# Performance work log

Measured on AMD Instinct MI355X. Metric: run time of the kernel, lower is better.

The kernel has to match this reference:

```python
import jax, jax.numpy as jnp
import numpy as np

N_NODES = 80000
N_EDGES = 1280000
N_GRAPHS = 256
NEG_SLOPE = 0.2


def _edge_softmax(alpha, dst, n):
    # PyG softmax over incoming edges per target node, with 1e-16 eps
    m = jax.ops.segment_max(alpha, dst, num_segments=n)          # [N,H]
    e = jnp.exp(alpha - m[dst])
    s = jax.ops.segment_sum(e, dst, num_segments=n)              # [N,H]
    return e / (s[dst] + 1e-16)


def _gat_layer(x, src, dst, W, a_src, a_dst, b, heads, out_ch):
    n = x.shape[0]
    h = (x @ W).reshape(n, heads, out_ch)                        # [N,H,C]
    al_src = (h * a_src).sum(-1)                                 # [N,H]
    al_dst = (h * a_dst).sum(-1)                                 # [N,H]
    alpha = jax.nn.leaky_relu(al_src[src] + al_dst[dst], NEG_SLOPE)  # [E,H]
    alpha = _edge_softmax(alpha, dst, n)
    out = jax.ops.segment_sum(h[src] * alpha[:, :, None], dst, num_segments=n)
    return out.reshape(n, heads * out_ch) + b


def setup_inputs() -> dict:
    key = jax.random.key(0)
    ks = jax.random.split(key, 16)
    x = jax.random.normal(ks[0], (N_NODES, 9), dtype=jnp.float32)
    edge_index = jax.random.randint(ks[1], (2, N_EDGES), 0, N_NODES, dtype=jnp.int64)
    batch = jnp.sort(jax.random.randint(ks[2], (N_NODES,), 0, N_GRAPHS, dtype=jnp.int64))
    s = 0.1
    p = {}
    p['W1'] = jax.random.normal(ks[3], (9, 3 * 45), dtype=jnp.float32) * s
    p['a_src1'] = jax.random.normal(ks[4], (3, 45), dtype=jnp.float32) * s
    p['a_dst1'] = jax.random.normal(ks[5], (3, 45), dtype=jnp.float32) * s
    p['b1'] = jnp.zeros((3 * 45,), dtype=jnp.float32)
    p['W2'] = jax.random.normal(ks[6], (135, 3 * 18), dtype=jnp.float32) * s
    p['a_src2'] = jax.random.normal(ks[7], (3, 18), dtype=jnp.float32) * s
    p['a_dst2'] = jax.random.normal(ks[8], (3, 18), dtype=jnp.float32) * s
    p['b2'] = jnp.zeros((3 * 18,), dtype=jnp.float32)
    p['W3'] = jax.random.normal(ks[9], (54, 4), dtype=jnp.float32) * s
    p['a_src3'] = jax.random.normal(ks[10], (1, 4), dtype=jnp.float32) * s
    p['a_dst3'] = jax.random.normal(ks[11], (1, 4), dtype=jnp.float32) * s
    p['b3'] = jnp.zeros((4,), dtype=jnp.float32)
    return dict(x=x, edge_index=edge_index, batch=batch, **p)


def reference(x, edge_index, batch,
              W1, a_src1, a_dst1, b1,
              W2, a_src2, a_dst2, b2,
              W3, a_src3, a_dst3, b3):
    n = x.shape[0]
    # GATConv default: add self-loops once (same structure every layer)
    loop = jnp.arange(n, dtype=edge_index.dtype)
    src = jnp.concatenate([edge_index[0], loop])
    dst = jnp.concatenate([edge_index[1], loop])

    h = _gat_layer(x, src, dst, W1, a_src1, a_dst1, b1, 3, 45)
    h = jax.nn.relu(h)  # dropout is identity in eval mode
    h = _gat_layer(h, src, dst, W2, a_src2, a_dst2, b2, 3, 18)
    h = jax.nn.relu(h)
    h = _gat_layer(h, src, dst, W3, a_src3, a_dst3, b3, 1, 4)

    g = jax.ops.segment_max(h, batch, num_segments=N_GRAPHS)  # global_max_pool
    g = jnp.where(jnp.isneginf(g), jnp.float32(-1e9), g)      # guard empty graphs
    return jax.nn.log_softmax(g, axis=1)
```

## Files before the change

### kernel.cpp

```cpp
#include <hip/hip_runtime.h>
#include <hip/hip_bf16.h>

#define N_NODES 80000
#define N_EDGES 1280000
#define E_TOT   (N_EDGES + N_NODES)
#define N_GRAPHS 256
#define NEG_SLOPE 0.2f

__device__ __forceinline__ float leaky(float a) { return fmaxf(a, NEG_SLOPE * a); }

template <int H>
__device__ __forceinline__ float pick(const float (&arr)[H], int h) {
    float r = arr[0];
    #pragma unroll
    for (int j = 1; j < H; ++j) r = (h == j) ? arr[j] : r;
    return r;
}

__device__ __forceinline__ unsigned f2mono(float f) {
    unsigned u = __float_as_uint(f);
    return u ^ ((u >> 31) ? 0xFFFFFFFFu : 0x80000000u);
}
__device__ __forceinline__ float mono2f(unsigned u) {
    u = (u & 0x80000000u) ? (u ^ 0x80000000u) : ~u;
    return __uint_as_float(u);
}

__global__ void k_init(int* __restrict__ counts, int* __restrict__ fill,
                       unsigned* __restrict__ genc) {
    int i = blockIdx.x * blockDim.x + threadIdx.x;
    if (i < N_NODES) { counts[i] = 0; fill[i] = 0; }
    if (i < N_GRAPHS * 4) genc[i] = f2mono(-1e9f);
}

__global__ void k_hist(const int* __restrict__ dst, int* __restrict__ counts) {
    int i = blockIdx.x * blockDim.x + threadIdx.x;
    if (i >= E_TOT) return;
    int d = (i < N_EDGES) ? dst[i] : (i - N_EDGES);
    atomicAdd(&counts[d], 1);
}

#define SCAN_B 256
__global__ void k_scan_block(const int* __restrict__ counts, int* __restrict__ rp,
                             int* __restrict__ bsum, int n) {
    __shared__ int sa[SCAN_B], sb[SCAN_B];
    int tid = threadIdx.x;
    int gi = blockIdx.x * SCAN_B + tid;
    int v = (gi < n) ? counts[gi] : 0;
    sa[tid] = v;
    __syncthreads();
    int* cur = sa; int* nxt = sb;
    #pragma unroll
    for (int d = 1; d < SCAN_B; d <<= 1) {
        int t = cur[tid];
        if (tid >= d) t += cur[tid - d];
        nxt[tid] = t;
        __syncthreads();
        int* tmp = cur; cur = nxt; nxt = tmp;
    }
    if (gi < n) rp[gi] = cur[tid] - v;
    if (tid == SCAN_B - 1) bsum[blockIdx.x] = cur[tid];
}

__global__ void k_scan_tops(const int* __restrict__ bsum, int* __restrict__ boff, int nb) {
    __shared__ int sa[512], sb[512];
    int tid = threadIdx.x;
    int v = (tid < nb) ? bsum[tid] : 0;
    sa[tid] = v;
    __syncthreads();
    int* cur = sa; int* nxt = sb;
    #pragma unroll
    for (int d = 1; d < 512; d <<= 1) {
        int t = cur[tid];
        if (tid >= d) t += cur[tid - d];
        nxt[tid] = t;
        __syncthreads();
        int* tmp = cur; cur = nxt; nxt = tmp;
    }
    if (tid < nb) boff[tid] = cur[tid] - v;
}

__global__ void k_scan_add_pre1(int* __restrict__ rp, const int* __restrict__ boff,
                                const float* __restrict__ x, const float* __restrict__ W1,
                                const float* __restrict__ as1, const float* __restrict__ ad1,
                                float* __restrict__ als, float* __restrict__ ald, int n) {
    __shared__ float ps[27], pd[27];
    int t = threadIdx.x;
    int gi = blockIdx.x * blockDim.x + t;
    if (gi < n) rp[gi] += boff[blockIdx.x];
    if (gi == 0) rp[n] = E_TOT;
    if (t < 27) {
        int h = t / 9, k = t % 9;
        float s = 0.f, d = 0.f;
        for (int c = 0; c < 45; ++c) {
            float w = W1[k * 135 + h * 45 + c];
            s += w * as1[h * 45 + c];
            d += w * ad1[h * 45 + c];
        }
        ps[t] = s; pd[t] = d;
    }
    __syncthreads();
    if (gi >= n) return;
    float xr[9];
    #pragma unroll
    for (int k = 0; k < 9; ++k) xr[k] = x[gi * 9 + k];
    #pragma unroll
    for (int h = 0; h < 3; ++h) {
        float s = 0.f, d = 0.f;
        #pragma unroll
        for (int k = 0; k < 9; ++k) { s += xr[k] * ps[h * 9 + k]; d += xr[k] * pd[h * 9 + k]; }
        als[gi * 3 + h] = s;
        ald[gi * 3 + h] = d;
    }
}

__global__ void k_scatter(const int* __restrict__ src, const int* __restrict__ dst,
                          const int* __restrict__ rp, int* __restrict__ fill,
                          int* __restrict__ srcs) {
    int i = blockIdx.x * blockDim.x + threadIdx.x;
    if (i >= E_TOT) return;
    int s, d;
    if (i < N_EDGES) { s = src[i]; d = dst[i]; }
    else             { s = i - N_EDGES; d = s; }
    int pos = rp[d] + atomicAdd(&fill[d], 1);
    srcs[pos] = s;
}

__global__ void k_agg1x(const int* __restrict__ rp, const int* __restrict__ srcs,
                        const float* __restrict__ x, const float* __restrict__ als,
                        const float* __restrict__ ald, float* __restrict__ wv,
                        float* __restrict__ aggx, int n) {
    int wid = threadIdx.x >> 6, lane = threadIdx.x & 63;
    int node = blockIdx.x * (blockDim.x >> 6) + wid;
    if (node >= n) return;
    int beg = rp[node], end = rp[node + 1];

    float aldv[3];
    #pragma unroll
    for (int h = 0; h < 3; ++h) aldv[h] = ald[node * 3 + h];

    float ss[3] = {0.f, 0.f, 0.f};
    for (int i = beg + lane; i < end; i += 64) {
        int s = srcs[i];
        #pragma unroll
        for (int h = 0; h < 3; ++h) {
            float e = __expf(leaky(als[s * 3 + h] + aldv[h]));
            wv[i * 3 + h] = e;
            ss[h] += e;
        }
    }
    #pragma unroll
    for (int h = 0; h < 3; ++h) {
        #pragma unroll
        for (int off = 32; off; off >>= 1) ss[h] += __shfl_xor(ss[h], off, 64);
    }
    float inv[3];
    #pragma unroll
    for (int h = 0; h < 3; ++h) inv[h] = 1.f / (ss[h] + 1e-16f);

    int es = lane >> 5, li = lane & 31;
    int lic = li < 27 ? li : 26;
    int hh = lic / 9;
    int kk = lic % 9;
    float invh = pick(inv, hh);

    float acc = 0.f;
    int i = beg + es;
    for (; i + 14 < end; i += 16) {
        int s0 = srcs[i],      s1 = srcs[i + 2],  s2 = srcs[i + 4],  s3 = srcs[i + 6];
        int s4 = srcs[i + 8],  s5 = srcs[i + 10], s6 = srcs[i + 12], s7 = srcs[i + 14];
        float w0 = wv[i * 3 + hh],        w1 = wv[(i + 2) * 3 + hh];
        float w2 = wv[(i + 4) * 3 + hh],  w3 = wv[(i + 6) * 3 + hh];
        float w4 = wv[(i + 8) * 3 + hh],  w5 = wv[(i + 10) * 3 + hh];
        float w6 = wv[(i + 12) * 3 + hh], w7 = wv[(i + 14) * 3 + hh];
        float x0 = x[s0 * 9 + kk], x1 = x[s1 * 9 + kk];
        float x2 = x[s2 * 9 + kk], x3 = x[s3 * 9 + kk];
        float x4 = x[s4 * 9 + kk], x5 = x[s5 * 9 + kk];
        float x6 = x[s6 * 9 + kk], x7 = x[s7 * 9 + kk];
        acc += x0 * w0 + x1 * w1 + x2 * w2 + x3 * w3
             + x4 * w4 + x5 * w5 + x6 * w6 + x7 * w7;
    }
    for (; i < end; i += 2) {
        acc += x[srcs[i] * 9 + kk] * wv[i * 3 + hh];
    }
    acc += __shfl_xor(acc, 32, 64);
    if (lane < 27) aggx[node * 27 + lane] = acc * invh;
}

__global__ void k_lin2f(const float* __restrict__ aggx, const float* __restrict__ W1,
                        const float* __restrict__ b1, const float* __restrict__ W2,
                        const float* __restrict__ as2, const float* __restrict__ ad2,
                        float* __restrict__ h2, float* __restrict__ als,
                        float* __restrict__ ald, int n) {
    int node = blockIdx.x * blockDim.x + threadIdx.x;
    if (node >= n) return;
    float ax[27];
    #pragma unroll
    for (int j = 0; j < 27; ++j) ax[j] = aggx[node * 27 + j];
    float acc[54];
    #pragma unroll
    for (int c = 0; c < 54; ++c) acc[c] = 0.f;
    #pragma unroll
    for (int h = 0; h < 3; ++h) {
        #pragma unroll 1
        for (int c0 = 0; c0 < 45; ++c0) {
            int col = h * 45 + c0;
            float t = b1[col];
            #pragma unroll
            for (int k = 0; k < 9; ++k) t += ax[h * 9 + k] * W1[k * 135 + col];
            t = fmaxf(t, 0.f);
            #pragma unroll
            for (int cc = 0; cc < 54; ++cc) acc[cc] += t * W2[col * 54 + cc];
        }
    }
    float as_[3] = {0.f, 0.f, 0.f}, ad_[3] = {0.f, 0.f, 0.f};
    #pragma unroll
    for (int c = 0; c < 54; ++c) {
        h2[node * 54 + c] = acc[c];
        as_[c / 18] += acc[c] * as2[c];
        ad_[c / 18] += acc[c] * ad2[c];
    }
    #pragma unroll
    for (int h = 0; h < 3; ++h) { als[node * 3 + h] = as_[h]; ald[node * 3 + h] = ad_[h]; }
}

__global__ void k_agg2(const int* __restrict__ rp, const int* __restrict__ srcs,
                       const float* __restrict__ h, const float* __restrict__ als,
                       const float* __restrict__ ald, float* __restrict__ wv,
                       const float* __restrict__ bias, float* __restrict__ out, int n) {
    int wid = threadIdx.x >> 6, lane = threadIdx.x & 63;
    int node = blockIdx.x * (blockDim.x >> 6) + wid;
    if (node >= n) return;
    int beg = rp[node], end = rp[node + 1];

    float aldv[3];
    #pragma unroll
    for (int hh = 0; hh < 3; ++hh) aldv[hh] = ald[node * 3 + hh];

    float ss[3] = {0.f, 0.f, 0.f};
    for (int i = beg + lane; i < end; i += 64) {
        int s = srcs[i];
        #pragma unroll
        for (int hh = 0; hh < 3; ++hh) {
            float e = __expf(leaky(als[s * 3 + hh] + aldv[hh]));
            wv[i * 3 + hh] = e;
            ss[hh] += e;
        }
    }
    #pragma unroll
    for (int hh = 0; hh < 3; ++hh) {
        #pragma unroll
        for (int off = 32; off; off >>= 1) ss[hh] += __shfl_xor(ss[hh], off, 64);
    }
    float inv[3];
    #pragma unroll
    for (int hh = 0; hh < 3; ++hh) inv[hh] = 1.f / (ss[hh] + 1e-16f);

    int es = lane >> 5, li = lane & 31;
    bool act = li < 27;
    int lic = act ? li : 26;
    int hh = lic / 9;
    float invh = pick(inv, hh);
    const float2* hv = (const float2*)h;

    float accx = 0.f, accy = 0.f;
    int i = beg + es;
    for (; i + 14 < end; i += 16) {
        int s0 = srcs[i],      s1 = srcs[i + 2],  s2 = srcs[i + 4],  s3 = srcs[i + 6];
        int s4 = srcs[i + 8],  s5 = srcs[i + 10], s6 = srcs[i + 12], s7 = srcs[i + 14];
        float w0 = wv[i * 3 + hh],        w1 = wv[(i + 2) * 3 + hh];
        float w2 = wv[(i + 4) * 3 + hh],  w3 = wv[(i + 6) * 3 + hh];
        float w4 = wv[(i + 8) * 3 + hh],  w5 = wv[(i + 10) * 3 + hh];
        float w6 = wv[(i + 12) * 3 + hh], w7 = wv[(i + 14) * 3 + hh];
        float2 v0 = hv[s0 * 27 + lic], v1 = hv[s1 * 27 + lic];
        float2 v2 = hv[s2 * 27 + lic], v3 = hv[s3 * 27 + lic];
        float2 v4 = hv[s4 * 27 + lic], v5 = hv[s5 * 27 + lic];
        float2 v6 = hv[s6 * 27 + lic], v7 = hv[s7 * 27 + lic];
        accx += v0.x * w0 + v1.x * w1 + v2.x * w2 + v3.x * w3
              + v4.x * w4 + v5.x * w5 + v6.x * w6 + v7.x * w7;
        accy += v0.y * w0 + v1.y * w1 + v2.y * w2 + v3.y * w3
              + v4.y * w4 + v5.y * w5 + v6.y * w6 + v7.y * w7;
    }
    for (; i < end; i += 2) {
        float w = wv[i * 3 + hh];
        float2 v = hv[srcs[i] * 27 + lic];
        accx += v.x * w;
        accy += v.y * w;
    }
    accx += __shfl_xor(accx, 32, 64);
    accy += __shfl_xor(accy, 32, 64);
    if (act && es == 0) {
        float2 b = ((const float2*)bias)[li];
        float2 o; o.x = accx * invh + b.x; o.y = accy * invh + b.y;
        ((float2*)out)[(long)node * 27 + li] = o;
    }
}

__global__ void k_lin3f(const float* __restrict__ out2, const float* __restrict__ W3,
                        const float* __restrict__ as3, const float* __restrict__ ad3,
                        float* __restrict__ h3, float* __restrict__ als,
                        float* __restrict__ ald, int n) {
    int node = blockIdx.x * blockDim.x + threadIdx.x;
    if (node >= n) return;
    float a0 = 0.f, a1 = 0.f, a2 = 0.f, a3 = 0.f;
    #pragma unroll 1
    for (int c = 0; c < 54; ++c) {
        float t = fmaxf(out2[node * 54 + c], 0.f);
        a0 += t * W3[c * 4 + 0];
        a1 += t * W3[c * 4 + 1];
        a2 += t * W3[c * 4 + 2];
        a3 += t * W3[c * 4 + 3];
    }
    h3[node * 4 + 0] = a0; h3[node * 4 + 1] = a1;
    h3[node * 4 + 2] = a2; h3[node * 4 + 3] = a3;
    als[node] = a0 * as3[0] + a1 * as3[1] + a2 * as3[2] + a3 * as3[3];
    ald[node] = a0 * ad3[0] + a1 * ad3[1] + a2 * ad3[2] + a3 * ad3[3];
}

__global__ void k_agg3pool(const int* __restrict__ rp, const int* __restrict__ srcs,
                           const float* __restrict__ h3, const float* __restrict__ als,
                           const float* __restrict__ ald, const float* __restrict__ b3,
                           const int* __restrict__ batch, unsigned* __restrict__ genc, int n) {
    int sub = threadIdx.x & 15;
    int node = blockIdx.x * (blockDim.x >> 4) + (threadIdx.x >> 4);
    if (node >= n) return;
    int beg = rp[node], end = rp[node + 1];
    float aldv = ald[node];

    float ss = 0.f;
    for (int i = beg + sub; i < end; i += 16)
        ss += __expf(leaky(als[srcs[i]] + aldv));
    #pragma unroll
    for (int off = 8; off; off >>= 1) ss += __shfl_xor(ss, off, 64);
    float inv = 1.f / (ss + 1e-16f);

    float ax = 0.f, ay = 0.f, az = 0.f, aw = 0.f;
    const float4* h4 = (const float4*)h3;
    for (int i = beg + sub; i < end; i += 16) {
        int s = srcs[i];
        float w = __expf(leaky(als[s] + aldv));
        float4 v = h4[s];
        ax += v.x * w; ay += v.y * w; az += v.z * w; aw += v.w * w;
    }
    #pragma unroll
    for (int off = 8; off; off >>= 1) {
        ax += __shfl_xor(ax, off, 64);
        ay += __shfl_xor(ay, off, 64);
        az += __shfl_xor(az, off, 64);
        aw += __shfl_xor(aw, off, 64);
    }
    if (sub < 4) {
        float v = (sub == 0) ? ax : (sub == 1) ? ay : (sub == 2) ? az : aw;
        atomicMax(&genc[batch[node] * 4 + sub], f2mono(v * inv + b3[sub]));
    }
}

__global__ void k_final(const unsigned* __restrict__ genc, float* __restrict__ out) {
    int g = threadIdx.x;
    float v[4];
    #pragma unroll
    for (int c = 0; c < 4; ++c) v[c] = mono2f(genc[g * 4 + c]);
    float mx = fmaxf(fmaxf(v[0], v[1]), fmaxf(v[2], v[3]));
    float s = 0.f;
    #pragma unroll
    for (int c = 0; c < 4; ++c) s += expf(v[c] - mx);
    float l = mx + logf(s);
    #pragma unroll
    for (int c = 0; c < 4; ++c) out[g * 4 + c] = v[c] - l;
}

extern "C" void kernel_launch(void* const* d_in, const int* in_sizes, int n_in,
                              void* d_out, int out_size, void* d_ws, size_t ws_size,
                              hipStream_t stream) {
    const float* x     = (const float*)d_in[0];
    const int*   ei    = (const int*)d_in[1];
    const int*   batch = (const int*)d_in[2];
    const float* W1    = (const float*)d_in[3];
    const float* as1   = (const float*)d_in[4];
    const float* ad1   = (const float*)d_in[5];
    const float* b1    = (const float*)d_in[6];
    const float* W2    = (const float*)d_in[7];
    const float* as2   = (const float*)d_in[8];
    const float* ad2   = (const float*)d_in[9];
    const float* b2    = (const float*)d_in[10];
    const float* W3    = (const float*)d_in[11];
    const float* as3   = (const float*)d_in[12];
    const float* ad3   = (const float*)d_in[13];
    const float* b3    = (const float*)d_in[14];
    float* out = (float*)d_out;

    const int* src = ei;
    const int* dst = ei + N_EDGES;

    char* base = (char*)d_ws;
    size_t off = 0;
    auto alloc = [&](size_t bytes) -> char* {
        char* p = base + off;
        off = (off + bytes + 255) & ~(size_t)255;
        return p;
    };
    int*      counts  = (int*)alloc((size_t)N_NODES * 4);
    int*      fill    = (int*)alloc((size_t)N_NODES * 4);
    int*      row_ptr = (int*)alloc((size_t)(N_NODES + 1) * 4);
    int*      srcs    = (int*)alloc((size_t)E_TOT * 4);
    int*      bsum    = (int*)alloc(512 * 4);
    int*      boff    = (int*)alloc(512 * 4);
    float*    als     = (float*)alloc((size_t)N_NODES * 3 * 4);
    float*    ald     = (float*)alloc((size_t)N_NODES * 3 * 4);
    float*    wv      = (float*)alloc((size_t)E_TOT * 3 * 4);
    float*    aggx    = (float*)alloc((size_t)N_NODES * 27 * 4);
    float*    h2      = (float*)alloc((size_t)N_NODES * 54 * 4);
    float*    out2    = (float*)alloc((size_t)N_NODES * 54 * 4);
    float*    h3      = (float*)alloc((size_t)N_NODES * 4 * 4);
    unsigned* genc    = (unsigned*)alloc((size_t)N_GRAPHS * 4 * 4);
    if (off > ws_size) return;

    const int TB = 256;
    const int nb_n  = (N_NODES + TB - 1) / TB;
    const int nb_et = (E_TOT + TB - 1) / TB;
    const int nb_w  = (N_NODES + 3) / 4;
    const int nb_16 = (N_NODES + 15) / 16;

    k_init<<<nb_n, TB, 0, stream>>>(counts, fill, genc);
    k_hist<<<nb_et, TB, 0, stream>>>(dst, counts);
    k_scan_block<<<nb_n, SCAN_B, 0, stream>>>(counts, row_ptr, bsum, N_NODES);
    k_scan_tops<<<1, 512, 0, stream>>>(bsum, boff, nb_n);
    k_scan_add_pre1<<<nb_n, TB, 0, stream>>>(row_ptr, boff, x, W1, as1, ad1, als, ald, N_NODES);
    k_scatter<<<nb_et, TB, 0, stream>>>(src, dst, row_ptr, fill, srcs);

    k_agg1x<<<nb_w, TB, 0, stream>>>(row_ptr, srcs, x, als, ald, wv, aggx, N_NODES);

    k_lin2f<<<nb_n, TB, 0, stream>>>(aggx, W1, b1, W2, as2, ad2, h2, als, ald, N_NODES);
    k_agg2<<<nb_w, TB, 0, stream>>>(row_ptr, srcs, h2, als, ald, wv, b2, out2, N_NODES);

    k_lin3f<<<nb_n, TB, 0, stream>>>(out2, W3, as3, ad3, h3, als, ald, N_NODES);
    k_agg3pool<<<nb_16, TB, 0, stream>>>(row_ptr, srcs, h3, als, ald, b3, batch, genc, N_NODES);
    k_final<<<1, N_GRAPHS, 0, stream>>>(genc, out);
}
```

Before: 547.0 us.

## Record edge ranks during histogram, store layer-2 features in fp16, fuse layer-3 linear into agg2

The histogram kernel now records each edge's atomic rank, so the scatter no longer needs a second atomic pass. Self-loops are placed at the first slot of each row during the scan-add step. Layer-2 features are stored as half2, which halves the gather traffic in agg2. The layer-3 linear projection and its attention logits are fused into agg2 through wave reductions, which removes the separate lin3 kernel and the out2 round trip. The cost is an extra erank buffer and reduced precision on the h2 features.

```diff
diff --git a/kernel.cpp b/kernel.cpp
--- a/kernel.cpp
+++ b/kernel.cpp
@@ -1,5 +1,6 @@
 #include <hip/hip_runtime.h>
 #include <hip/hip_bf16.h>
+#include <hip/hip_fp16.h>
 
 #define N_NODES 80000
 #define N_EDGES 1280000
@@ -26,18 +27,17 @@
     return __uint_as_float(u);
 }
 
-__global__ void k_init(int* __restrict__ counts, int* __restrict__ fill,
-                       unsigned* __restrict__ genc) {
+__global__ void k_init(int* __restrict__ counts, unsigned* __restrict__ genc) {
     int i = blockIdx.x * blockDim.x + threadIdx.x;
-    if (i < N_NODES) { counts[i] = 0; fill[i] = 0; }
+    if (i < N_NODES) counts[i] = 1;
     if (i < N_GRAPHS * 4) genc[i] = f2mono(-1e9f);
 }
 
-__global__ void k_hist(const int* __restrict__ dst, int* __restrict__ counts) {
+__global__ void k_hist(const int* __restrict__ dst, int* __restrict__ counts,
+                       int* __restrict__ erank) {
     int i = blockIdx.x * blockDim.x + threadIdx.x;
-    if (i >= E_TOT) return;
-    int d = (i < N_EDGES) ? dst[i] : (i - N_EDGES);
-    atomicAdd(&counts[d], 1);
+    if (i >= N_EDGES) return;
+    erank[i] = atomicAdd(&counts[dst[i]], 1);
 }
 
 #define SCAN_B 256
@@ -81,13 +81,18 @@
 }
 
 __global__ void k_scan_add_pre1(int* __restrict__ rp, const int* __restrict__ boff,
+                                int* __restrict__ srcs,
                                 const float* __restrict__ x, const float* __restrict__ W1,
                                 const float* __restrict__ as1, const float* __restrict__ ad1,
                                 float* __restrict__ als, float* __restrict__ ald, int n) {
     __shared__ float ps[27], pd[27];
     int t = threadIdx.x;
     int gi = blockIdx.x * blockDim.x + t;
-    if (gi < n) rp[gi] += boff[blockIdx.x];
+    if (gi < n) {
+        int r = rp[gi] + boff[blockIdx.x];
+        rp[gi] = r;
+        srcs[r] = gi;
+    }
     if (gi == 0) rp[n] = E_TOT;
     if (t < 27) {
         int h = t / 9, k = t % 9;
@@ -115,15 +120,11 @@
 }
 
 __global__ void k_scatter(const int* __restrict__ src, const int* __restrict__ dst,
-                          const int* __restrict__ rp, int* __restrict__ fill,
+                          const int* __restrict__ rp, const int* __restrict__ erank,
                           int* __restrict__ srcs) {
     int i = blockIdx.x * blockDim.x + threadIdx.x;
-    if (i >= E_TOT) return;
-    int s, d;
-    if (i < N_EDGES) { s = src[i]; d = dst[i]; }
-    else             { s = i - N_EDGES; d = s; }
-    int pos = rp[d] + atomicAdd(&fill[d], 1);
-    srcs[pos] = s;
+    if (i >= N_EDGES) return;
+    srcs[rp[dst[i]] + erank[i]] = src[i];
 }
 
 __global__ void k_agg1x(const int* __restrict__ rp, const int* __restrict__ srcs,
@@ -190,7 +191,7 @@
 __global__ void k_lin2f(const float* __restrict__ aggx, const float* __restrict__ W1,
                         const float* __restrict__ b1, const float* __restrict__ W2,
                         const float* __restrict__ as2, const float* __restrict__ ad2,
-                        float* __restrict__ h2, float* __restrict__ als,
+                        __half2* __restrict__ h2, float* __restrict__ als,
                         float* __restrict__ ald, int n) {
     int node = blockIdx.x * blockDim.x + threadIdx.x;
     if (node >= n) return;
@@ -216,18 +217,23 @@
     float as_[3] = {0.f, 0.f, 0.f}, ad_[3] = {0.f, 0.f, 0.f};
     #pragma unroll
     for (int c = 0; c < 54; ++c) {
-        h2[node * 54 + c] = acc[c];
         as_[c / 18] += acc[c] * as2[c];
         ad_[c / 18] += acc[c] * ad2[c];
     }
     #pragma unroll
+    for (int j = 0; j < 27; ++j)
+        h2[node * 27 + j] = __floats2half2_rn(acc[2 * j], acc[2 * j + 1]);
+    #pragma unroll
     for (int h = 0; h < 3; ++h) { als[node * 3 + h] = as_[h]; ald[node * 3 + h] = ad_[h]; }
 }
 
 __global__ void k_agg2(const int* __restrict__ rp, const int* __restrict__ srcs,
-                       const float* __restrict__ h, const float* __restrict__ als,
+                       const __half2* __restrict__ hv, const float* __restrict__ als,
                        const float* __restrict__ ald, float* __restrict__ wv,
-                       const float* __restrict__ bias, float* __restrict__ out, int n) {
+                       const float* __restrict__ bias, const float* __restrict__ W3,
+                       const float* __restrict__ as3, const float* __restrict__ ad3,
+                       float* __restrict__ h3, float* __restrict__ als3,
+                       float* __restrict__ ald3, int n) {
     int wid = threadIdx.x >> 6, lane = threadIdx.x & 63;
     int node = blockIdx.x * (blockDim.x >> 6) + wid;
     if (node >= n) return;
@@ -261,7 +267,6 @@
     int lic = act ? li : 26;
     int hh = lic / 9;
     float invh = pick(inv, hh);
-    const float2* hv = (const float2*)h;
 
     float accx = 0.f, accy = 0.f;
     int i = beg + es;
@@ -272,10 +277,10 @@
         float w2 = wv[(i + 4) * 3 + hh],  w3 = wv[(i + 6) * 3 + hh];
         float w4 = wv[(i + 8) * 3 + hh],  w5 = wv[(i + 10) * 3 + hh];
         float w6 = wv[(i + 12) * 3 + hh], w7 = wv[(i + 14) * 3 + hh];
-        float2 v0 = hv[s0 * 27 + lic], v1 = hv[s1 * 27 + lic];
-        float2 v2 = hv[s2 * 27 + lic], v3 = hv[s3 * 27 + lic];
-        float2 v4 = hv[s4 * 27 + lic], v5 = hv[s5 * 27 + lic];
-        float2 v6 = hv[s6 * 27 + lic], v7 = hv[s7 * 27 + lic];
+        float2 v0 = __half22float2(hv[s0 * 27 + lic]), v1 = __half22float2(hv[s1 * 27 + lic]);
+        float2 v2 = __half22float2(hv[s2 * 27 + lic]), v3 = __half22float2(hv[s3 * 27 + lic]);
+        float2 v4 = __half22float2(hv[s4 * 27 + lic]), v5 = __half22float2(hv[s5 * 27 + lic]);
+        float2 v6 = __half22float2(hv[s6 * 27 + lic]), v7 = __half22float2(hv[s7 * 27 + lic]);
         accx += v0.x * w0 + v1.x * w1 + v2.x * w2 + v3.x * w3
               + v4.x * w4 + v5.x * w5 + v6.x * w6 + v7.x * w7;
         accy += v0.y * w0 + v1.y * w1 + v2.y * w2 + v3.y * w3
@@ -283,53 +288,52 @@
     }
     for (; i < end; i += 2) {
         float w = wv[i * 3 + hh];
-        float2 v = hv[srcs[i] * 27 + lic];
+        float2 v = __half22float2(hv[srcs[i] * 27 + lic]);
         accx += v.x * w;
         accy += v.y * w;
     }
     accx += __shfl_xor(accx, 32, 64);
     accy += __shfl_xor(accy, 32, 64);
-    if (act && es == 0) {
-        float2 b = ((const float2*)bias)[li];
-        float2 o; o.x = accx * invh + b.x; o.y = accy * invh + b.y;
-        ((float2*)out)[(long)node * 27 + li] = o;
-    }
-}
-
-__global__ void k_lin3f(const float* __restrict__ out2, const float* __restrict__ W3,
-                        const float* __restrict__ as3, const float* __restrict__ ad3,
-                        float* __restrict__ h3, float* __restrict__ als,
-                        float* __restrict__ ald, int n) {
-    int node = blockIdx.x * blockDim.x + threadIdx.x;
-    if (node >= n) return;
-    float a0 = 0.f, a1 = 0.f, a2 = 0.f, a3 = 0.f;
-    #pragma unroll 1
-    for (int c = 0; c < 54; ++c) {
-        float t = fmaxf(out2[node * 54 + c], 0.f);
-        a0 += t * W3[c * 4 + 0];
-        a1 += t * W3[c * 4 + 1];
-        a2 += t * W3[c * 4 + 2];
-        a3 += t * W3[c * 4 + 3];
-    }
-    h3[node * 4 + 0] = a0; h3[node * 4 + 1] = a1;
-    h3[node * 4 + 2] = a2; h3[node * 4 + 3] = a3;
-    als[node] = a0 * as3[0] + a1 * as3[1] + a2 * as3[2] + a3 * as3[3];
-    ald[node] = a0 * ad3[0] + a1 * ad3[1] + a2 * ad3[2] + a3 * ad3[3];
+
+    float p0 = 0.f, p1 = 0.f, p2 = 0.f, p3 = 0.f;
+    if (act) {
+        float2 b = ((const float2*)bias)[lic];
+        float r0 = fmaxf(accx * invh + b.x, 0.f);
+        float r1 = fmaxf(accy * invh + b.y, 0.f);
+        int c0 = 2 * lic, c1 = 2 * lic + 1;
+        p0 = r0 * W3[c0 * 4 + 0] + r1 * W3[c1 * 4 + 0];
+        p1 = r0 * W3[c0 * 4 + 1] + r1 * W3[c1 * 4 + 1];
+        p2 = r0 * W3[c0 * 4 + 2] + r1 * W3[c1 * 4 + 2];
+        p3 = r0 * W3[c0 * 4 + 3] + r1 * W3[c1 * 4 + 3];
+    }
+    #pragma unroll
+    for (int off = 16; off; off >>= 1) {
+        p0 += __shfl_xor(p0, off, 64);
+        p1 += __shfl_xor(p1, off, 64);
+        p2 += __shfl_xor(p2, off, 64);
+        p3 += __shfl_xor(p3, off, 64);
+    }
+    if (lane == 0) {
+        float4 o; o.x = p0; o.y = p1; o.z = p2; o.w = p3;
+        ((float4*)h3)[node] = o;
+        als3[node] = p0 * as3[0] + p1 * as3[1] + p2 * as3[2] + p3 * as3[3];
+        ald3[node] = p0 * ad3[0] + p1 * ad3[1] + p2 * ad3[2] + p3 * ad3[3];
+    }
 }
 
 __global__ void k_agg3pool(const int* __restrict__ rp, const int* __restrict__ srcs,
-                           const float* __restrict__ h3, const float* __restrict__ als,
-                           const float* __restrict__ ald, const float* __restrict__ b3,
+                           const float* __restrict__ h3, const float* __restrict__ als3,
+                           const float* __restrict__ ald3, const float* __restrict__ b3,
                            const int* __restrict__ batch, unsigned* __restrict__ genc, int n) {
     int sub = threadIdx.x & 15;
     int node = blockIdx.x * (blockDim.x >> 4) + (threadIdx.x >> 4);
     if (node >= n) return;
     int beg = rp[node], end = rp[node + 1];
-    float aldv = ald[node];
+    float aldv = ald3[node];
 
     float ss = 0.f;
     for (int i = beg + sub; i < end; i += 16)
-        ss += __expf(leaky(als[srcs[i]] + aldv));
+        ss += __expf(leaky(als3[srcs[i]] + aldv));
     #pragma unroll
     for (int off = 8; off; off >>= 1) ss += __shfl_xor(ss, off, 64);
     float inv = 1.f / (ss + 1e-16f);
@@ -338,7 +342,7 @@
     const float4* h4 = (const float4*)h3;
     for (int i = beg + sub; i < end; i += 16) {
         int s = srcs[i];
-        float w = __expf(leaky(als[s] + aldv));
+        float w = __expf(leaky(als3[s] + aldv));
         float4 v = h4[s];
         ax += v.x * w; ay += v.y * w; az += v.z * w; aw += v.w * w;
     }
@@ -400,40 +404,41 @@
         return p;
     };
     int*      counts  = (int*)alloc((size_t)N_NODES * 4);
-    int*      fill    = (int*)alloc((size_t)N_NODES * 4);
     int*      row_ptr = (int*)alloc((size_t)(N_NODES + 1) * 4);
     int*      srcs    = (int*)alloc((size_t)E_TOT * 4);
+    int*      erank   = (int*)alloc((size_t)N_EDGES * 4);
     int*      bsum    = (int*)alloc(512 * 4);
     int*      boff    = (int*)alloc(512 * 4);
     float*    als     = (float*)alloc((size_t)N_NODES * 3 * 4);
     float*    ald     = (float*)alloc((size_t)N_NODES * 3 * 4);
+    float*    als3    = (float*)alloc((size_t)N_NODES * 4);
+    float*    ald3    = (float*)alloc((size_t)N_NODES * 4);
     float*    wv      = (float*)alloc((size_t)E_TOT * 3 * 4);
     float*    aggx    = (float*)alloc((size_t)N_NODES * 27 * 4);
-    float*    h2      = (float*)alloc((size_t)N_NODES * 54 * 4);
-    float*    out2    = (float*)alloc((size_t)N_NODES * 54 * 4);
+    __half2*  h2      = (__half2*)alloc((size_t)N_NODES * 27 * 4);
     float*    h3      = (float*)alloc((size_t)N_NODES * 4 * 4);
     unsigned* genc    = (unsigned*)alloc((size_t)N_GRAPHS * 4 * 4);
     if (off > ws_size) return;
 
     const int TB = 256;
     const int nb_n  = (N_NODES + TB - 1) / TB;
-    const int nb_et = (E_TOT + TB - 1) / TB;
+    const int nb_e  = (N_EDGES + TB - 1) / TB;
     const int nb_w  = (N_NODES + 3) / 4;
     const int nb_16 = (N_NODES + 15) / 16;
 
-    k_init<<<nb_n, TB, 0, stream>>>(counts, fill, genc);
-    k_hist<<<nb_et, TB, 0, stream>>>(dst, counts);
+    k_init<<<nb_n, TB, 0, stream>>>(counts, genc);
+    k_hist<<<nb_e, TB, 0, stream>>>(dst, counts, erank);
     k_scan_block<<<nb_n, SCAN_B, 0, stream>>>(counts, row_ptr, bsum, N_NODES);
     k_scan_tops<<<1, 512, 0, stream>>>(bsum, boff, nb_n);
-    k_scan_add_pre1<<<nb_n, TB, 0, stream>>>(row_ptr, boff, x, W1, as1, ad1, als, ald, N_NODES);
-    k_scatter<<<nb_et, TB, 0, stream>>>(src, dst, row_ptr, fill, srcs);
+    k_scan_add_pre1<<<nb_n, TB, 0, stream>>>(row_ptr, boff, srcs, x, W1, as1, ad1, als, ald, N_NODES);
+    k_scatter<<<nb_e, TB, 0, stream>>>(src, dst, row_ptr, erank, srcs);
 
     k_agg1x<<<nb_w, TB, 0, stream>>>(row_ptr, srcs, x, als, ald, wv, aggx, N_NODES);
 
     k_lin2f<<<nb_n, TB, 0, stream>>>(aggx, W1, b1, W2, as2, ad2, h2, als, ald, N_NODES);
-    k_agg2<<<nb_w, TB, 0, stream>>>(row_ptr, srcs, h2, als, ald, wv, b2, out2, N_NODES);
-
-    k_lin3f<<<nb_n, TB, 0, stream>>>(out2, W3, as3, ad3, h3, als, ald, N_NODES);
-    k_agg3pool<<<nb_16, TB, 0, stream>>>(row_ptr, srcs, h3, als, ald, b3, batch, genc, N_NODES);
+    k_agg2<<<nb_w, TB, 0, stream>>>(row_ptr, srcs, h2, als, ald, wv, b2,
+                                    W3, as3, ad3, h3, als3, ald3, N_NODES);
+
+    k_agg3pool<<<nb_16, TB, 0, stream>>>(row_ptr, srcs, h3, als3, ald3, b3, batch, genc, N_NODES);
     k_final<<<1, N_GRAPHS, 0, stream>>>(genc, out);
 }
```

Measured after the change: 478.8 us. 12.5% less time.
